# Performance work log

Measured on AMD Instinct MI355X. Metric: run time of the kernel, lower is better.

Reference implementation:

```python
import jax, jax.numpy as jnp
import numpy as np

D_MODEL = 1024
N_HEAD = 16
D_FF = 4 * D_MODEL
LN_EPS = 1e-5


def _layernorm(x, g, b):
    mu = jnp.mean(x, axis=-1, keepdims=True)
    var = jnp.mean(jnp.square(x - mu), axis=-1, keepdims=True)
    return (x - mu) * jax.lax.rsqrt(var + LN_EPS) * g + b


def _mha(q_in, k_in, v_in, mask, wq, bq, wk, wv, bv, wo, bo):
    B, Tq, D = q_in.shape
    H, Dk = N_HEAD, D // N_HEAD
    q = (q_in @ wq + bq).reshape(B, Tq, H, Dk).transpose(0, 2, 1, 3)      # [B,H,Tq,Dk]
    k = (k_in @ wk).reshape(B, -1, H, Dk).transpose(0, 2, 1, 3)           # [B,H,Tk,Dk]
    v = (v_in @ wv + bv).reshape(B, -1, H, Dk).transpose(0, 2, 1, 3)      # [B,H,Tk,Dk]
    attn = jnp.einsum('bhqd,bhkd->bhqk', q, k) / jnp.sqrt(jnp.float32(Dk))
    if mask is not None:
        m0 = (mask[:, None, :, :] == 0)                                    # [B,1,Tq,Tk]
        attn = jnp.where(m0, -jnp.inf, attn)
        attn = jax.nn.softmax(attn, axis=-1)
        attn = jnp.where(m0, 0.0, attn)
    else:
        attn = jax.nn.softmax(attn, axis=-1)
    out = jnp.einsum('bhqk,bhkd->bhqd', attn, v)
    out = out.transpose(0, 2, 1, 3).reshape(B, Tq, D)
    return out @ wo + bo


def setup_inputs() -> dict:
    key = jax.random.key(0)
    ks = jax.random.split(key, 32)
    B, T, S, D = 4, 1024, 1024, D_MODEL
    w = lambda k, shp: 0.02 * jax.random.normal(k, shp, dtype=jnp.float32)
    inp = {
        'dec_input': jax.random.normal(ks[0], (B, T, D), dtype=jnp.float32),
        'enc_output': jax.random.normal(ks[1], (B, S, D), dtype=jnp.float32),
        'self_mask': jnp.broadcast_to(jnp.tril(jnp.ones((T, T), jnp.int32)), (B, T, T)),
        'cross_mask': jnp.ones((B, T, S), jnp.int32),
        'sa_ln_g': jnp.ones((D,), jnp.float32), 'sa_ln_b': jnp.zeros((D,), jnp.float32),
        'sa_wq': w(ks[2], (D, D)), 'sa_bq': jnp.zeros((D,), jnp.float32),
        'sa_wk': w(ks[3], (D, D)),
        'sa_wv': w(ks[4], (D, D)), 'sa_bv': jnp.zeros((D,), jnp.float32),
        'sa_wo': w(ks[5], (D, D)), 'sa_bo': jnp.zeros((D,), jnp.float32),
        'ca_ln_g': jnp.ones((D,), jnp.float32), 'ca_ln_b': jnp.zeros((D,), jnp.float32),
        'ca_wq': w(ks[6], (D, D)), 'ca_bq': jnp.zeros((D,), jnp.float32),
        'ca_wk': w(ks[7], (D, D)),
        'ca_wv': w(ks[8], (D, D)), 'ca_bv': jnp.zeros((D,), jnp.float32),
        'ca_wo': w(ks[9], (D, D)), 'ca_bo': jnp.zeros((D,), jnp.float32),
        'mlp_ln_g': jnp.ones((D,), jnp.float32), 'mlp_ln_b': jnp.zeros((D,), jnp.float32),
        'w1': w(ks[10], (D, D_FF)), 'b1': jnp.zeros((D_FF,), jnp.float32),
        'w2': w(ks[11], (D_FF, D)), 'b2': jnp.zeros((D,), jnp.float32),
    }
    return inp


def reference(dec_input, enc_output, self_mask, cross_mask,
              sa_ln_g, sa_ln_b, sa_wq, sa_bq, sa_wk, sa_wv, sa_bv, sa_wo, sa_bo,
              ca_ln_g, ca_ln_b, ca_wq, ca_bq, ca_wk, ca_wv, ca_bv, ca_wo, ca_bo,
              mlp_ln_g, mlp_ln_b, w1, b1, w2, b2):
    # self-attention block (pre-norm, residual)
    x = _layernorm(dec_input, sa_ln_g, sa_ln_b)
    x = dec_input + _mha(x, x, x, self_mask, sa_wq, sa_bq, sa_wk, sa_wv, sa_bv, sa_wo, sa_bo)
    # cross-attention block
    h = _layernorm(x, ca_ln_g, ca_ln_b)
    x = x + _mha(h, enc_output, enc_output, cross_mask, ca_wq, ca_bq, ca_wk, ca_wv, ca_bv, ca_wo, ca_bo)
    # GELU FFN block
    h = _layernorm(x, mlp_ln_g, mlp_ln_b)
    x = x + (jax.nn.gelu(h @ w1 + b1, approximate=False) @ w2 + b2)
    return x
```

## Files before the change

### kernel.cpp

```cpp
#include <hip/hip_runtime.h>
#include <math.h>

typedef unsigned short u16;
typedef unsigned int   u32;
typedef __attribute__((ext_vector_type(8))) short bf16x8;
typedef __attribute__((ext_vector_type(4))) float f32x4;

__device__ __forceinline__ u16 f2bf(float f) {
  u32 u = __builtin_bit_cast(u32, f);
  u += 0x7fffu + ((u >> 16) & 1u);
  return (u16)(u >> 16);
}
__device__ __forceinline__ u32 pack2(float a, float b) {
  return (u32)f2bf(a) | ((u32)f2bf(b) << 16);
}

__device__ __forceinline__ void g2l16(const u16* g, u16* l) {
  __builtin_amdgcn_global_load_lds(
      (const __attribute__((address_space(1))) unsigned int*)g,
      (__attribute__((address_space(3))) unsigned int*)l, 16, 0, 0);
}

struct TC8 { const float* s[8]; u16* d[8]; };
__global__ __launch_bounds__(256)
void transcvt8_kernel(TC8 p) {
  const float* __restrict__ W = p.s[blockIdx.z];
  u16* __restrict__ Wt = p.d[blockIdx.z];
  __shared__ float tile[32][33];
  const int n0 = blockIdx.x * 32, k0 = blockIdx.y * 32;
  const int tx = threadIdx.x & 31, ty = threadIdx.x >> 5;
  for (int i = 0; i < 4; ++i)
    tile[ty + 8 * i][tx] = W[(size_t)(k0 + ty + 8 * i) * 1024 + n0 + tx];
  __syncthreads();
  for (int i = 0; i < 4; ++i)
    Wt[(size_t)(n0 + ty + 8 * i) * 1024 + k0 + tx] = f2bf(tile[tx][ty + 8 * i]);
}

__global__ __launch_bounds__(256)
void transcvt_kernel(const float* __restrict__ W, u16* __restrict__ Wt, int K, int N) {
  __shared__ float tile[32][33];
  const int n0 = blockIdx.x * 32, k0 = blockIdx.y * 32;
  const int tx = threadIdx.x & 31, ty = threadIdx.x >> 5;
  for (int i = 0; i < 4; ++i)
    tile[ty + 8 * i][tx] = W[(size_t)(k0 + ty + 8 * i) * N + n0 + tx];
  __syncthreads();
  for (int i = 0; i < 4; ++i)
    Wt[(size_t)(n0 + ty + 8 * i) * K + k0 + tx] = f2bf(tile[tx][ty + 8 * i]);
}

__global__ __launch_bounds__(256)
void cvt_kernel(const float* __restrict__ in, u16* __restrict__ out) {
  const int i = blockIdx.x * 256 + threadIdx.x;
  const float4 v = ((const float4*)in)[i];
  u16 o[4] = {f2bf(v.x), f2bf(v.y), f2bf(v.z), f2bf(v.w)};
  ((ushort4*)out)[i] = *(ushort4*)o;
}

__global__ __launch_bounds__(256)
void pack_bias_kernel(const float* __restrict__ bq, const float* __restrict__ bv,
                      const float* __restrict__ cbv,
                      float* __restrict__ B3, float* __restrict__ B2) {
  const int i = blockIdx.x * 256 + threadIdx.x;
  if (i < 3072) {
    float v = 0.0f;
    if (i < 1024) v = bq[i];
    else if (i >= 2048) v = bv[i - 2048];
    B3[i] = v;
  } else {
    const int j = i - 3072;
    B2[j] = (j >= 1024) ? cbv[j - 1024] : 0.0f;
  }
}

__global__ __launch_bounds__(256)
void ln_kernel(const float* __restrict__ x, const float* __restrict__ g,
               const float* __restrict__ b, u16* __restrict__ out) {
  const int row = blockIdx.x;
  const float4 v4 = ((const float4*)(x + (size_t)row * 1024))[threadIdx.x];
  float vv[4] = {v4.x, v4.y, v4.z, v4.w};
  float s = vv[0] + vv[1] + vv[2] + vv[3];
  float s2 = vv[0] * vv[0] + vv[1] * vv[1] + vv[2] * vv[2] + vv[3] * vv[3];
  for (int m = 1; m < 64; m <<= 1) { s += __shfl_xor(s, m); s2 += __shfl_xor(s2, m); }
  __shared__ float ss[4], ss2[4];
  const int w = threadIdx.x >> 6;
  if ((threadIdx.x & 63) == 0) { ss[w] = s; ss2[w] = s2; }
  __syncthreads();
  s = ss[0] + ss[1] + ss[2] + ss[3];
  s2 = ss2[0] + ss2[1] + ss2[2] + ss2[3];
  const float mu = s * (1.0f / 1024.0f);
  const float var = s2 * (1.0f / 1024.0f) - mu * mu;
  const float r = rsqrtf(var + 1e-5f);
  const int c = threadIdx.x * 4;
  const float4 g4 = ((const float4*)g)[threadIdx.x];
  const float4 b4 = ((const float4*)b)[threadIdx.x];
  float gg[4] = {g4.x, g4.y, g4.z, g4.w};
  float bb[4] = {b4.x, b4.y, b4.z, b4.w};
  u16 o[4];
  for (int j = 0; j < 4; ++j) o[j] = f2bf((vv[j] - mu) * r * gg[j] + bb[j]);
  ((ushort4*)(out + (size_t)row * 1024 + c))[0] = *(ushort4*)o;
}

template<bool RES_F32, bool GELU>
__global__ __launch_bounds__(512)
void gemm_kernel(const u16* __restrict__ A, const u16* __restrict__ Bt,
                 const float* __restrict__ bias, const float* __restrict__ res,
                 void* __restrict__ Cout, int M, int N, int K) {
  __shared__ u16 As[2][128][32];
  __shared__ u16 Bs[2][128][32];
  const int t = threadIdx.x, lane = t & 63, w = t >> 6;
  const int wr = w >> 2, wc = w & 3;
  const int nwg = gridDim.x * gridDim.y;
  int bid = blockIdx.y * gridDim.x + blockIdx.x;
  bid = (bid & 7) * (nwg >> 3) + (bid >> 3);
  const int m0 = (bid / gridDim.x) * 128, n0 = (bid % gridDim.x) * 128;
  const int fr = lane & 15, fg = lane >> 4;
  const int srow = lane >> 2, scol = (lane & 3) * 8;
  const u16* Ag = &A[(size_t)(m0 + w * 16 + srow) * K + scol];
  const u16* Bg = &Bt[(size_t)(n0 + w * 16 + srow) * K + scol];
  f32x4 acc[4][2] = {};
  g2l16(Ag, &As[0][w * 16][0]);
  g2l16(Bg, &Bs[0][w * 16][0]);
  __syncthreads();
  int cur = 0;
  for (int k0 = 0; k0 < K; k0 += 32) {
    if (k0 + 32 < K) {
      const int nx = cur ^ 1, kn = k0 + 32;
      g2l16(Ag + kn, &As[nx][w * 16][0]);
      g2l16(Bg + kn, &Bs[nx][w * 16][0]);
    }
    bf16x8 af[4], bfr[2];
    for (int m = 0; m < 4; ++m) af[m] = *(bf16x8*)&As[cur][wr * 64 + m * 16 + fr][fg * 8];
    for (int n = 0; n < 2; ++n) bfr[n] = *(bf16x8*)&Bs[cur][wc * 32 + n * 16 + fr][fg * 8];
    __builtin_amdgcn_s_setprio(1);
    for (int m = 0; m < 4; ++m)
      for (int n = 0; n < 2; ++n)
        acc[m][n] = __builtin_amdgcn_mfma_f32_16x16x32_bf16(af[m], bfr[n], acc[m][n], 0, 0, 0);
    __builtin_amdgcn_s_setprio(0);
    __syncthreads();
    cur ^= 1;
  }
  for (int m = 0; m < 4; ++m)
    for (int n = 0; n < 2; ++n) {
      const int col = n0 + wc * 32 + n * 16 + fr;
      const float bv = bias ? bias[col] : 0.0f;
      for (int i = 0; i < 4; ++i) {
        const int row = m0 + wr * 64 + m * 16 + fg * 4 + i;
        float v = acc[m][n][i] + bv;
        if (GELU) v = 0.5f * v * (1.0f + erff(v * 0.70710678118654752f));
        if (RES_F32)
          ((float*)Cout)[(size_t)row * N + col] = res[(size_t)row * N + col] + v;
        else
          ((u16*)Cout)[(size_t)row * N + col] = f2bf(v);
      }
    }
}

template<bool CAUSAL>
__global__ __launch_bounds__(256)
void attn_kernel(const u16* __restrict__ Q, int ldq,
                 const u16* __restrict__ K, int ldk,
                 const u16* __restrict__ V, int ldv,
                 u16* __restrict__ O) {
  __shared__ u16 VsT[2][64][64];
  __shared__ u16 Ps[4][16][72];
  const int bh = blockIdx.y, b = bh >> 4, h = bh & 15;
  const int q0 = blockIdx.x * 64;
  const int t = threadIdx.x, w = t >> 6, lane = t & 63;
  const int ql = lane & 15;
  const int hi = lane >> 4;
  const int qr = q0 + w * 16;
  const int qz = qr + ql;
  const int hcol = h * 64;
  const size_t qgrow = (size_t)(b * 1024 + qz) * ldq + hcol;
  bf16x8 qb[2];
  qb[0] = *(const bf16x8*)&Q[qgrow + hi * 8];
  qb[1] = *(const bf16x8*)&Q[qgrow + 32 + hi * 8];
  f32x4 o[4] = {};
  float mrow = -1e30f;
  float lsum = 0.0f;
  const int sp = t >> 3, sm = t & 7;
  const float c1 = 0.125f * 1.44269504f;
  const int nkt = CAUSAL ? (blockIdx.x + 1) : 16;
  {
    const bf16x8 va = *(const bf16x8*)&V[(size_t)(b * 1024 + 2 * sp) * ldv + hcol + 8 * sm];
    const bf16x8 vb = *(const bf16x8*)&V[(size_t)(b * 1024 + 2 * sp + 1) * ldv + hcol + 8 * sm];
    #pragma unroll
    for (int jj = 0; jj < 8; ++jj) {
      u32 pr = (u32)((const u16*)&va)[jj] | ((u32)((const u16*)&vb)[jj] << 16);
      *(u32*)&VsT[0][8 * sm + jj][(2 * sp) ^ ((jj ^ sm) << 3)] = pr;
    }
  }
  __syncthreads();
  int cur = 0;
  for (int kt = 0; kt < nkt; ++kt) {
    const int k0 = kt * 64;
    bf16x8 va, vb;
    const bool havenext = (kt + 1 < nkt);
    if (havenext) {
      va = *(const bf16x8*)&V[(size_t)(b * 1024 + k0 + 64 + 2 * sp) * ldv + hcol + 8 * sm];
      vb = *(const bf16x8*)&V[(size_t)(b * 1024 + k0 + 64 + 2 * sp + 1) * ldv + hcol + 8 * sm];
    }
    f32x4 s[4] = {};
    #pragma unroll
    for (int kk = 0; kk < 2; ++kk) {
      bf16x8 kf[4];
      #pragma unroll
      for (int j = 0; j < 4; ++j)
        kf[j] = *(const bf16x8*)&K[(size_t)(b * 1024 + k0 + j * 16 + ql) * ldk + hcol + kk * 32 + hi * 8];
      __builtin_amdgcn_s_setprio(1);
      #pragma unroll
      for (int j = 0; j < 4; ++j)
        s[j] = __builtin_amdgcn_mfma_f32_16x16x32_bf16(kf[j], qb[kk], s[j], 0, 0, 0);
      __builtin_amdgcn_s_setprio(0);
    }
    float e2[4][4];
    float rm = -1e30f;
    const bool domask = CAUSAL && (kt == nkt - 1);
    #pragma unroll
    for (int j = 0; j < 4; ++j)
      #pragma unroll
      for (int i = 0; i < 4; ++i) {
        float a = s[j][i] * c1;
        if (domask && (k0 + j * 16 + hi * 4 + i > qz)) a = -1e30f;
        e2[j][i] = a;
        rm = fmaxf(rm, a);
      }
    if (!__all(rm <= mrow + 8.0f)) {
      rm = fmaxf(rm, __shfl_xor(rm, 16));
      rm = fmaxf(rm, __shfl_xor(rm, 32));
      const float mn = fmaxf(mrow, rm);
      const float sc = exp2f(mrow - mn);
      lsum *= sc;
      float scv[4];
      #pragma unroll
      for (int i = 0; i < 4; ++i) scv[i] = __shfl(sc, hi * 4 + i);
      #pragma unroll
      for (int nb = 0; nb < 4; ++nb)
        #pragma unroll
        for (int i = 0; i < 4; ++i) o[nb][i] *= scv[i];
      mrow = mn;
    }
    float p[4][4];
    #pragma unroll
    for (int j = 0; j < 4; ++j)
      #pragma unroll
      for (int i = 0; i < 4; ++i) { p[j][i] = exp2f(e2[j][i] - mrow); lsum += p[j][i]; }
    #pragma unroll
    for (int j = 0; j < 4; ++j) {
      *(u32*)&Ps[w][ql][j * 16 + hi * 4]     = pack2(p[j][0], p[j][1]);
      *(u32*)&Ps[w][ql][j * 16 + hi * 4 + 2] = pack2(p[j][2], p[j][3]);
    }
    asm volatile("s_waitcnt lgkmcnt(0)" ::: "memory");
    __builtin_amdgcn_sched_barrier(0);
    bf16x8 pa[2];
    pa[0] = *(const bf16x8*)&Ps[w][ql][hi * 8];
    pa[1] = *(const bf16x8*)&Ps[w][ql][32 + hi * 8];
    __builtin_amdgcn_s_setprio(1);
    #pragma unroll
    for (int nb = 0; nb < 4; ++nb) {
      const int dim = nb * 16 + ql;
      const int swz = ((dim & 7) ^ ((dim >> 3) & 7)) << 3;
      const bf16x8 v0 = *(const bf16x8*)&VsT[cur][dim][(hi * 8) ^ swz];
      const bf16x8 v1 = *(const bf16x8*)&VsT[cur][dim][(32 + hi * 8) ^ swz];
      o[nb] = __builtin_amdgcn_mfma_f32_16x16x32_bf16(pa[0], v0, o[nb], 0, 0, 0);
      o[nb] = __builtin_amdgcn_mfma_f32_16x16x32_bf16(pa[1], v1, o[nb], 0, 0, 0);
    }
    __builtin_amdgcn_s_setprio(0);
    if (havenext) {
      const int nx = cur ^ 1;
      #pragma unroll
      for (int jj = 0; jj < 8; ++jj) {
        u32 pr = (u32)((const u16*)&va)[jj] | ((u32)((const u16*)&vb)[jj] << 16);
        *(u32*)&VsT[nx][8 * sm + jj][(2 * sp) ^ ((jj ^ sm) << 3)] = pr;
      }
    }
    __syncthreads();
    cur ^= 1;
  }
  float ltot = lsum + __shfl_xor(lsum, 16);
  ltot += __shfl_xor(ltot, 32);
  const float inv = 1.0f / ltot;
  #pragma unroll
  for (int i = 0; i < 4; ++i) {
    const float invq = __shfl(inv, hi * 4 + i);
    const size_t row = (size_t)(b * 1024 + qr + hi * 4 + i);
    #pragma unroll
    for (int nb = 0; nb < 4; ++nb)
      O[row * 1024 + hcol + nb * 16 + ql] = f2bf(o[nb][i] * invq);
  }
}

extern "C" void kernel_launch(void* const* d_in, const int* in_sizes, int n_in,
                              void* d_out, int out_size, void* d_ws, size_t ws_size,
                              hipStream_t stream) {
  const float* dec  = (const float*)d_in[0];
  const float* enc  = (const float*)d_in[1];
  const float* sa_g = (const float*)d_in[4];
  const float* sa_b = (const float*)d_in[5];
  const float* sa_wq = (const float*)d_in[6];
  const float* sa_bq = (const float*)d_in[7];
  const float* sa_wk = (const float*)d_in[8];
  const float* sa_wv = (const float*)d_in[9];
  const float* sa_bv = (const float*)d_in[10];
  const float* sa_wo = (const float*)d_in[11];
  const float* sa_bo = (const float*)d_in[12];
  const float* ca_g = (const float*)d_in[13];
  const float* ca_b = (const float*)d_in[14];
  const float* ca_wq = (const float*)d_in[15];
  const float* ca_bq = (const float*)d_in[16];
  const float* ca_wk = (const float*)d_in[17];
  const float* ca_wv = (const float*)d_in[18];
  const float* ca_bv = (const float*)d_in[19];
  const float* ca_wo = (const float*)d_in[20];
  const float* ca_bo = (const float*)d_in[21];
  const float* mlp_g = (const float*)d_in[22];
  const float* mlp_b = (const float*)d_in[23];
  const float* w1 = (const float*)d_in[24];
  const float* b1 = (const float*)d_in[25];
  const float* w2 = (const float*)d_in[26];
  const float* b2 = (const float*)d_in[27];

  const size_t MB = 1024 * 1024;
  if (ws_size < 97 * MB) return;
  char* ws = (char*)d_ws;
  u16* WQKV = (u16*)(ws + 0 * MB);
  u16* CQT  = (u16*)(ws + 6 * MB);
  u16* CKV  = (u16*)(ws + 8 * MB);
  u16* WOT  = (u16*)(ws + 12 * MB);
  u16* COT  = (u16*)(ws + 14 * MB);
  float* B3 = (float*)(ws + 16 * MB);
  float* B2 = (float*)(ws + 16 * MB + 16384);
  u16* XLN  = (u16*)(ws + 17 * MB);
  u16* AO   = (u16*)(ws + 25 * MB);
  u16* W1T  = (u16*)(ws + 25 * MB);
  u16* ENC  = (u16*)(ws + 33 * MB);
  u16* FB   = (u16*)(ws + 41 * MB);
  u16* EF   = (u16*)(ws + 41 * MB);
  u16* CQB  = (u16*)(ws + 57 * MB);
  u16* H1   = (u16*)(ws + 33 * MB);
  float* X1 = (float*)(ws + 65 * MB);
  u16* W2T  = (u16*)(ws + 65 * MB);
  float* X2 = (float*)(ws + 81 * MB);
  float* OUT = (float*)d_out;

  const dim3 blk(256), gblk(512);
  TC8 tc;
  tc.s[0] = sa_wq; tc.d[0] = WQKV;
  tc.s[1] = sa_wk; tc.d[1] = WQKV + 1024 * 1024;
  tc.s[2] = sa_wv; tc.d[2] = WQKV + 2048 * 1024;
  tc.s[3] = sa_wo; tc.d[3] = WOT;
  tc.s[4] = ca_wq; tc.d[4] = CQT;
  tc.s[5] = ca_wk; tc.d[5] = CKV;
  tc.s[6] = ca_wv; tc.d[6] = CKV + 1024 * 1024;
  tc.s[7] = ca_wo; tc.d[7] = COT;
  transcvt8_kernel<<<dim3(32, 32, 8), blk, 0, stream>>>(tc);
  pack_bias_kernel<<<dim3(20), blk, 0, stream>>>(sa_bq, sa_bv, ca_bv, B3, B2);
  cvt_kernel<<<dim3(4096), blk, 0, stream>>>(enc, ENC);

  ln_kernel<<<dim3(4096), blk, 0, stream>>>(dec, sa_g, sa_b, XLN);
  gemm_kernel<false, false><<<dim3(24, 32), gblk, 0, stream>>>(XLN, WQKV, B3, nullptr, FB, 4096, 3072, 1024);
  attn_kernel<true><<<dim3(16, 64), blk, 0, stream>>>(FB, 3072, FB + 1024, 3072, FB + 2048, 3072, AO);
  gemm_kernel<true, false><<<dim3(8, 32), gblk, 0, stream>>>(AO, WOT, sa_bo, dec, X1, 4096, 1024, 1024);

  ln_kernel<<<dim3(4096), blk, 0, stream>>>(X1, ca_g, ca_b, XLN);
  gemm_kernel<false, false><<<dim3(16, 32), gblk, 0, stream>>>(ENC, CKV, B2, nullptr, EF, 4096, 2048, 1024);
  gemm_kernel<false, false><<<dim3(8, 32), gblk, 0, stream>>>(XLN, CQT, ca_bq, nullptr, CQB, 4096, 1024, 1024);
  attn_kernel<false><<<dim3(16, 64), blk, 0, stream>>>(CQB, 1024, EF, 2048, EF + 1024, 2048, AO);
  gemm_kernel<true, false><<<dim3(8, 32), gblk, 0, stream>>>(AO, COT, ca_bo, X1, X2, 4096, 1024, 1024);

  transcvt_kernel<<<dim3(128, 32), blk, 0, stream>>>(w1, W1T, 1024, 4096);
  transcvt_kernel<<<dim3(32, 128), blk, 0, stream>>>(w2, W2T, 4096, 1024);
  ln_kernel<<<dim3(4096), blk, 0, stream>>>(X2, mlp_g, mlp_b, XLN);
  gemm_kernel<false, true><<<dim3(32, 32), gblk, 0, stream>>>(XLN, W1T, b1, nullptr, H1, 4096, 4096, 1024);
  gemm_kernel<true, false><<<dim3(8, 32), gblk, 0, stream>>>(H1, W2T, b2, X2, OUT, 4096, 1024, 4096);
}
```

Measured before the change: 454.1 us.

## Double the attention query tile, register-prefetch K, use hardware bf16 pack

The attention kernel now runs 512 threads (8 waves) over a 128-row query tile, so each staged V tile is shared by twice as many waves. K fragments are prefetched into registers one key tile ahead through a ping-ponged body lambda. The grid is reordered so batch-heads run along x, and in the causal case each wave skips key tiles past its own diagonal. The software bf16 round-and-pack is replaced with the v_cvt_pk_bf16_f32 instruction; this costs more registers per wave and adds idle waves at block-wide syncs in the causal case.

After: 451.5 us. No clear change (-0.6%).

```diff
diff --git a/kernel.cpp b/kernel.cpp
--- a/kernel.cpp
+++ b/kernel.cpp
@@ -11,8 +11,10 @@
   u += 0x7fffu + ((u >> 16) & 1u);
   return (u16)(u >> 16);
 }
-__device__ __forceinline__ u32 pack2(float a, float b) {
-  return (u32)f2bf(a) | ((u32)f2bf(b) << 16);
+__device__ __forceinline__ u32 cvtpk(float lo, float hi_) {
+  u32 r;
+  asm("v_cvt_pk_bf16_f32 %0, %1, %2" : "=v"(r) : "v"(lo), "v"(hi_));
+  return r;
 }
 
 __device__ __forceinline__ void g2l16(const u16* g, u16* l) {
@@ -156,118 +158,129 @@
 }
 
 template<bool CAUSAL>
-__global__ __launch_bounds__(256)
+__global__ __launch_bounds__(512)
 void attn_kernel(const u16* __restrict__ Q, int ldq,
                  const u16* __restrict__ K, int ldk,
                  const u16* __restrict__ V, int ldv,
                  u16* __restrict__ O) {
   __shared__ u16 VsT[2][64][64];
-  __shared__ u16 Ps[4][16][72];
-  const int bh = blockIdx.y, b = bh >> 4, h = bh & 15;
-  const int q0 = blockIdx.x * 64;
+  __shared__ u16 Ps[8][16][72];
+  const int bh = blockIdx.x, b = bh >> 4, h = bh & 15;
+  const int qy = blockIdx.y;
   const int t = threadIdx.x, w = t >> 6, lane = t & 63;
   const int ql = lane & 15;
   const int hi = lane >> 4;
-  const int qr = q0 + w * 16;
+  const int qr = qy * 128 + w * 16;
   const int qz = qr + ql;
   const int hcol = h * 64;
+  const int nkt = CAUSAL ? 2 * qy + 2 : 16;
+  const int wlim = CAUSAL ? (qr >> 6) : nkt - 1;
+  const u16* Kb = K + (size_t)(b * 1024) * ldk + hcol;
+  const u16* Vb = V + (size_t)(b * 1024) * ldv + hcol;
   const size_t qgrow = (size_t)(b * 1024 + qz) * ldq + hcol;
-  bf16x8 qb[2];
-  qb[0] = *(const bf16x8*)&Q[qgrow + hi * 8];
-  qb[1] = *(const bf16x8*)&Q[qgrow + 32 + hi * 8];
+  const bf16x8 qb0 = *(const bf16x8*)&Q[qgrow + hi * 8];
+  const bf16x8 qb1 = *(const bf16x8*)&Q[qgrow + 32 + hi * 8];
   f32x4 o[4] = {};
-  float mrow = -1e30f;
-  float lsum = 0.0f;
+  float mrow = -1e30f, lsum = 0.0f;
   const int sp = t >> 3, sm = t & 7;
   const float c1 = 0.125f * 1.44269504f;
-  const int nkt = CAUSAL ? (blockIdx.x + 1) : 16;
-  {
-    const bf16x8 va = *(const bf16x8*)&V[(size_t)(b * 1024 + 2 * sp) * ldv + hcol + 8 * sm];
-    const bf16x8 vb = *(const bf16x8*)&V[(size_t)(b * 1024 + 2 * sp + 1) * ldv + hcol + 8 * sm];
+  if (t < 256) {
+    const bf16x8 va = *(const bf16x8*)&Vb[(size_t)(2 * sp) * ldv + 8 * sm];
+    const bf16x8 vb = *(const bf16x8*)&Vb[(size_t)(2 * sp + 1) * ldv + 8 * sm];
     #pragma unroll
     for (int jj = 0; jj < 8; ++jj) {
       u32 pr = (u32)((const u16*)&va)[jj] | ((u32)((const u16*)&vb)[jj] << 16);
       *(u32*)&VsT[0][8 * sm + jj][(2 * sp) ^ ((jj ^ sm) << 3)] = pr;
     }
   }
-  __syncthreads();
-  int cur = 0;
-  for (int kt = 0; kt < nkt; ++kt) {
+  bf16x8 kA[8], kB[8];
+  #pragma unroll
+  for (int j = 0; j < 4; ++j) {
+    kA[j]     = *(const bf16x8*)&Kb[(size_t)(j * 16 + ql) * ldk + hi * 8];
+    kA[4 + j] = *(const bf16x8*)&Kb[(size_t)(j * 16 + ql) * ldk + 32 + hi * 8];
+  }
+  __syncthreads();
+
+  auto body = [&](bf16x8 (&kc)[8], bf16x8 (&kn)[8], const int kt) {
     const int k0 = kt * 64;
     bf16x8 va, vb;
-    const bool havenext = (kt + 1 < nkt);
-    if (havenext) {
-      va = *(const bf16x8*)&V[(size_t)(b * 1024 + k0 + 64 + 2 * sp) * ldv + hcol + 8 * sm];
-      vb = *(const bf16x8*)&V[(size_t)(b * 1024 + k0 + 64 + 2 * sp + 1) * ldv + hcol + 8 * sm];
-    }
-    f32x4 s[4] = {};
-    #pragma unroll
-    for (int kk = 0; kk < 2; ++kk) {
-      bf16x8 kf[4];
+    const bool stageV = (kt + 1 < nkt) && (t < 256);
+    if (stageV) {
+      va = *(const bf16x8*)&Vb[(size_t)(k0 + 64 + 2 * sp) * ldv + 8 * sm];
+      vb = *(const bf16x8*)&Vb[(size_t)(k0 + 64 + 2 * sp + 1) * ldv + 8 * sm];
+    }
+    if (kt + 1 <= wlim) {
+      #pragma unroll
+      for (int j = 0; j < 4; ++j) {
+        kn[j]     = *(const bf16x8*)&Kb[(size_t)(k0 + 64 + j * 16 + ql) * ldk + hi * 8];
+        kn[4 + j] = *(const bf16x8*)&Kb[(size_t)(k0 + 64 + j * 16 + ql) * ldk + 32 + hi * 8];
+      }
+    }
+    if (kt <= wlim) {
+      f32x4 s[4] = {};
+      __builtin_amdgcn_s_setprio(1);
       #pragma unroll
       for (int j = 0; j < 4; ++j)
-        kf[j] = *(const bf16x8*)&K[(size_t)(b * 1024 + k0 + j * 16 + ql) * ldk + hcol + kk * 32 + hi * 8];
+        s[j] = __builtin_amdgcn_mfma_f32_16x16x32_bf16(kc[j], qb0, s[j], 0, 0, 0);
+      #pragma unroll
+      for (int j = 0; j < 4; ++j)
+        s[j] = __builtin_amdgcn_mfma_f32_16x16x32_bf16(kc[4 + j], qb1, s[j], 0, 0, 0);
+      __builtin_amdgcn_s_setprio(0);
+      float e2[4][4];
+      float rm = -1e30f;
+      const bool domask = CAUSAL && (kt == wlim);
+      #pragma unroll
+      for (int j = 0; j < 4; ++j)
+        #pragma unroll
+        for (int i = 0; i < 4; ++i) {
+          float a = s[j][i] * c1;
+          if (domask && (k0 + j * 16 + hi * 4 + i > qz)) a = -1e30f;
+          e2[j][i] = a;
+          rm = fmaxf(rm, a);
+        }
+      if (!__all(rm <= mrow + 8.0f)) {
+        rm = fmaxf(rm, __shfl_xor(rm, 16));
+        rm = fmaxf(rm, __shfl_xor(rm, 32));
+        const float mn = fmaxf(mrow, rm);
+        const float sc = exp2f(mrow - mn);
+        lsum *= sc;
+        float scv[4];
+        #pragma unroll
+        for (int i = 0; i < 4; ++i) scv[i] = __shfl(sc, hi * 4 + i);
+        #pragma unroll
+        for (int nb = 0; nb < 4; ++nb)
+          #pragma unroll
+          for (int i = 0; i < 4; ++i) o[nb][i] *= scv[i];
+        mrow = mn;
+      }
+      float p[4][4];
+      #pragma unroll
+      for (int j = 0; j < 4; ++j)
+        #pragma unroll
+        for (int i = 0; i < 4; ++i) { p[j][i] = exp2f(e2[j][i] - mrow); lsum += p[j][i]; }
+      #pragma unroll
+      for (int j = 0; j < 4; ++j) {
+        *(u32*)&Ps[w][ql][j * 16 + hi * 4]     = cvtpk(p[j][0], p[j][1]);
+        *(u32*)&Ps[w][ql][j * 16 + hi * 4 + 2] = cvtpk(p[j][2], p[j][3]);
+      }
+      asm volatile("s_waitcnt lgkmcnt(0)" ::: "memory");
+      __builtin_amdgcn_sched_barrier(0);
+      const bf16x8 pa0 = *(const bf16x8*)&Ps[w][ql][hi * 8];
+      const bf16x8 pa1 = *(const bf16x8*)&Ps[w][ql][32 + hi * 8];
       __builtin_amdgcn_s_setprio(1);
       #pragma unroll
-      for (int j = 0; j < 4; ++j)
-        s[j] = __builtin_amdgcn_mfma_f32_16x16x32_bf16(kf[j], qb[kk], s[j], 0, 0, 0);
+      for (int nb = 0; nb < 4; ++nb) {
+        const int dim = nb * 16 + ql;
+        const int swz = ((dim & 7) ^ ((dim >> 3) & 7)) << 3;
+        const bf16x8 v0 = *(const bf16x8*)&VsT[kt & 1][dim][(hi * 8) ^ swz];
+        const bf16x8 v1 = *(const bf16x8*)&VsT[kt & 1][dim][(32 + hi * 8) ^ swz];
+        o[nb] = __builtin_amdgcn_mfma_f32_16x16x32_bf16(pa0, v0, o[nb], 0, 0, 0);
+        o[nb] = __builtin_amdgcn_mfma_f32_16x16x32_bf16(pa1, v1, o[nb], 0, 0, 0);
+      }
       __builtin_amdgcn_s_setprio(0);
     }
-    float e2[4][4];
-    float rm = -1e30f;
-    const bool domask = CAUSAL && (kt == nkt - 1);
-    #pragma unroll
-    for (int j = 0; j < 4; ++j)
-      #pragma unroll
-      for (int i = 0; i < 4; ++i) {
-        float a = s[j][i] * c1;
-        if (domask && (k0 + j * 16 + hi * 4 + i > qz)) a = -1e30f;
-        e2[j][i] = a;
-        rm = fmaxf(rm, a);
-      }
-    if (!__all(rm <= mrow + 8.0f)) {
-      rm = fmaxf(rm, __shfl_xor(rm, 16));
-      rm = fmaxf(rm, __shfl_xor(rm, 32));
-      const float mn = fmaxf(mrow, rm);
-      const float sc = exp2f(mrow - mn);
-      lsum *= sc;
-      float scv[4];
-      #pragma unroll
-      for (int i = 0; i < 4; ++i) scv[i] = __shfl(sc, hi * 4 + i);
-      #pragma unroll
-      for (int nb = 0; nb < 4; ++nb)
-        #pragma unroll
-        for (int i = 0; i < 4; ++i) o[nb][i] *= scv[i];
-      mrow = mn;
-    }
-    float p[4][4];
-    #pragma unroll
-    for (int j = 0; j < 4; ++j)
-      #pragma unroll
-      for (int i = 0; i < 4; ++i) { p[j][i] = exp2f(e2[j][i] - mrow); lsum += p[j][i]; }
-    #pragma unroll
-    for (int j = 0; j < 4; ++j) {
-      *(u32*)&Ps[w][ql][j * 16 + hi * 4]     = pack2(p[j][0], p[j][1]);
-      *(u32*)&Ps[w][ql][j * 16 + hi * 4 + 2] = pack2(p[j][2], p[j][3]);
-    }
-    asm volatile("s_waitcnt lgkmcnt(0)" ::: "memory");
-    __builtin_amdgcn_sched_barrier(0);
-    bf16x8 pa[2];
-    pa[0] = *(const bf16x8*)&Ps[w][ql][hi * 8];
-    pa[1] = *(const bf16x8*)&Ps[w][ql][32 + hi * 8];
-    __builtin_amdgcn_s_setprio(1);
-    #pragma unroll
-    for (int nb = 0; nb < 4; ++nb) {
-      const int dim = nb * 16 + ql;
-      const int swz = ((dim & 7) ^ ((dim >> 3) & 7)) << 3;
-      const bf16x8 v0 = *(const bf16x8*)&VsT[cur][dim][(hi * 8) ^ swz];
-      const bf16x8 v1 = *(const bf16x8*)&VsT[cur][dim][(32 + hi * 8) ^ swz];
-      o[nb] = __builtin_amdgcn_mfma_f32_16x16x32_bf16(pa[0], v0, o[nb], 0, 0, 0);
-      o[nb] = __builtin_amdgcn_mfma_f32_16x16x32_bf16(pa[1], v1, o[nb], 0, 0, 0);
-    }
-    __builtin_amdgcn_s_setprio(0);
-    if (havenext) {
-      const int nx = cur ^ 1;
+    if (stageV) {
+      const int nx = (kt & 1) ^ 1;
       #pragma unroll
       for (int jj = 0; jj < 8; ++jj) {
         u32 pr = (u32)((const u16*)&va)[jj] | ((u32)((const u16*)&vb)[jj] << 16);
@@ -275,8 +288,13 @@
       }
     }
     __syncthreads();
-    cur ^= 1;
-  }
+  };
+
+  for (int kt = 0; kt < nkt; kt += 2) {
+    body(kA, kB, kt);
+    if (kt + 1 < nkt) body(kB, kA, kt + 1);
+  }
+
   float ltot = lsum + __shfl_xor(lsum, 16);
   ltot += __shfl_xor(ltot, 32);
   const float inv = 1.0f / ltot;
@@ -343,7 +361,7 @@
   float* X2 = (float*)(ws + 81 * MB);
   float* OUT = (float*)d_out;
 
-  const dim3 blk(256), gblk(512);
+  const dim3 blk(256), gblk(512), ablk(512);
   TC8 tc;
   tc.s[0] = sa_wq; tc.d[0] = WQKV;
   tc.s[1] = sa_wk; tc.d[1] = WQKV + 1024 * 1024;
@@ -359,13 +377,13 @@
 
   ln_kernel<<<dim3(4096), blk, 0, stream>>>(dec, sa_g, sa_b, XLN);
   gemm_kernel<false, false><<<dim3(24, 32), gblk, 0, stream>>>(XLN, WQKV, B3, nullptr, FB, 4096, 3072, 1024);
-  attn_kernel<true><<<dim3(16, 64), blk, 0, stream>>>(FB, 3072, FB + 1024, 3072, FB + 2048, 3072, AO);
+  attn_kernel<true><<<dim3(64, 8), ablk, 0, stream>>>(FB, 3072, FB + 1024, 3072, FB + 2048, 3072, AO);
   gemm_kernel<true, false><<<dim3(8, 32), gblk, 0, stream>>>(AO, WOT, sa_bo, dec, X1, 4096, 1024, 1024);
 
   ln_kernel<<<dim3(4096), blk, 0, stream>>>(X1, ca_g, ca_b, XLN);
   gemm_kernel<false, false><<<dim3(16, 32), gblk, 0, stream>>>(ENC, CKV, B2, nullptr, EF, 4096, 2048, 1024);
   gemm_kernel<false, false><<<dim3(8, 32), gblk, 0, stream>>>(XLN, CQT, ca_bq, nullptr, CQB, 4096, 1024, 1024);
-  attn_kernel<false><<<dim3(16, 64), blk, 0, stream>>>(CQB, 1024, EF, 2048, EF + 1024, 2048, AO);
+  attn_kernel<false><<<dim3(64, 8), ablk, 0, stream>>>(CQB, 1024, EF, 2048, EF + 1024, 2048, AO);
   gemm_kernel<true, false><<<dim3(8, 32), gblk, 0, stream>>>(AO, COT, ca_bo, X1, X2, 4096, 1024, 1024);
 
   transcvt_kernel<<<dim3(128, 32), blk, 0, stream>>>(w1, W1T, 1024, 4096);
```
